# Kernel tuning notes

Hardware: AMD Instinct MI355X
Metric: run time of the kernel (lower is better)

The kernel has to match this reference:

```python
import jax, jax.numpy as jnp
import numpy as np
import math

N = 2048; L = 100; D_IN = 128; D_STATE = 16; D_INNER = 256
MAMBA_DIM = 128; GAT_HID = 64; HEADS = 4; GAT_OUT = 64


def _lin(key, fin, fout, scale=0.02):
    k1, k2 = jax.random.split(key)
    return (jax.random.normal(k1, (fin, fout), jnp.float32) * scale,
            jnp.zeros((fout,), jnp.float32))


def setup_inputs() -> dict:
    key = jax.random.key(0)
    ks = jax.random.split(key, 16)
    temporal_data = jax.random.normal(ks[0], (N, L, D_IN), jnp.float32)
    graph_x = jax.random.normal(ks[1], (N, D_IN), jnp.float32)
    adj = (jax.random.uniform(ks[2], (N, N)) < 0.005).astype(jnp.float32)
    adj_matrix = jnp.maximum(adj, jnp.eye(N, dtype=jnp.float32))
    pos_emb = jax.random.normal(ks[3], (1, 100, D_IN), jnp.float32)
    Wi, bi = _lin(ks[4], D_IN, D_INNER)
    Wg, bg = _lin(ks[5], D_IN, D_INNER)
    A_log = jnp.linspace(math.log(1e-3), math.log(0.1), D_STATE).reshape(1, D_STATE).astype(jnp.float32)
    Wb, bb = _lin(ks[6], D_INNER, D_STATE)
    Wc, bc = _lin(ks[7], D_IN, D_STATE)
    Wo, bo = _lin(ks[8], D_INNER, D_IN)
    Wfc, bfc = _lin(ks[9], D_IN, MAMBA_DIM)
    W1 = jax.random.normal(ks[10], (HEADS, D_IN, GAT_HID), jnp.float32) * 0.05
    a1 = jax.random.normal(ks[11], (HEADS, 2 * GAT_HID), jnp.float32) * 0.05
    W2 = jax.random.normal(ks[12], (1, HEADS * GAT_HID, GAT_OUT), jnp.float32) * 0.05
    a2 = jax.random.normal(ks[13], (1, 2 * GAT_OUT), jnp.float32) * 0.05
    return dict(temporal_data=temporal_data, graph_x=graph_x, adj_matrix=adj_matrix,
                pos_emb=pos_emb, Wi=Wi, bi=bi, Wg=Wg, bg=bg, A_log=A_log,
                Wb=Wb, bb=bb, Wc=Wc, bc=bc, Wo=Wo, bo=bo, Wfc=Wfc, bfc=bfc,
                W1=W1, a1=a1, W2=W2, a2=a2)


def _mamba(x, pos_emb, Wi, bi, Wg, bg, A_log, Wb, bb, Wc, bc, Wo, bo):
    Bt, Ls, _ = x.shape
    x = x + pos_emb[:, :Ls, :]
    x_gated = (x @ Wi + bi) * jax.nn.sigmoid(x @ Wg + bg)   # [B,L,d_inner]
    Bmat = x_gated @ Wb + bb                                 # [B,L,d_state]
    Cmat = x @ Wc + bc                                       # [B,L,d_state]
    A = jnp.exp(0.01 * jnp.exp(A_log))                       # [1,d_state] (dt=0.01)

    def step(h, bc):
        b, c = bc
        h = A * h + b
        return h, h * c

    h0 = jnp.zeros((Bt, A_log.shape[1]), x.dtype)
    _, ys = jax.lax.scan(step, h0, (jnp.swapaxes(Bmat, 0, 1), jnp.swapaxes(Cmat, 0, 1)))
    y = jnp.swapaxes(ys, 0, 1)                               # [B,L,d_state]
    d_inner = Wo.shape[0]
    out_exp = jnp.concatenate(
        [y, jnp.zeros((Bt, Ls, d_inner - y.shape[-1]), x.dtype)], axis=-1)
    return out_exp @ Wo + bo


def _gat_layer(x, adj, W, a, concat):
    # x: [N,Fin], W: [H,Fin,Fout], a: [H,2*Fout]
    F_out = W.shape[2]
    xt = jnp.einsum('nf,hfo->hno', x, W)                     # [H,N,Fout]
    e_src = jnp.einsum('hno,ho->hn', xt, a[:, :F_out])       # a . x_i part
    e_dst = jnp.einsum('hno,ho->hn', xt, a[:, F_out:])       # a . x_j part
    e = jax.nn.leaky_relu(e_src[:, :, None] + e_dst[:, None, :], 0.2)
    e = jnp.where(adj[None, :, :] > 0, e, -jnp.inf)
    att = jax.nn.softmax(e, axis=2)                          # masked entries -> 0
    h_prime = jnp.einsum('hij,hjo->hio', att, xt)            # [H,N,Fout]
    if concat:
        return jnp.transpose(h_prime, (1, 0, 2)).reshape(x.shape[0], -1)
    return h_prime.mean(axis=0)


def reference(temporal_data, graph_x, adj_matrix, pos_emb, Wi, bi, Wg, bg, A_log,
              Wb, bb, Wc, bc, Wo, bo, Wfc, bfc, W1, a1, W2, a2):
    mamba_out = _mamba(temporal_data, pos_emb, Wi, bi, Wg, bg, A_log, Wb, bb, Wc, bc, Wo, bo)
    mamba_features = mamba_out @ Wfc + bfc
    # GAT stack (dropout is identity in eval mode)
    h = _gat_layer(graph_x, adj_matrix, W1, a1, concat=True)
    h = jax.nn.relu(h)
    gat_features = _gat_layer(h, adj_matrix, W2, a2, concat=False)
    return mamba_features, gat_features
```

## Files before the change

kernel.cpp:

```cpp
#include <hip/hip_runtime.h>
#include <hip/hip_bf16.h>

#define N_NODES 2048
#define L_SEQ   100
#define ROWS    (N_NODES * L_SEQ)
#define HEADS   4
#define GHID    64

typedef __attribute__((ext_vector_type(8))) short bf16x8;
typedef __attribute__((ext_vector_type(4))) float floatx4;

__device__ __forceinline__ short f2bf(float f) {
    union { float f; unsigned u; } v; v.f = f;
    return (short)((v.u + 0x8000u) >> 16);
}

constexpr size_t OFF_WCOMB = 0;
constexpr size_t OFF_BCOMB = 2048;
constexpr size_t OFF_AEXP  = 2176;
constexpr size_t OFF_WIGS  = 2192;
constexpr size_t OFF_WBS   = 34960;
constexpr size_t OFF_WCS   = 37008;
constexpr size_t OFF_BM    = 38032;
constexpr size_t OFF_CM    = OFF_BM + (size_t)ROWS * 16;
constexpr size_t OFF_GAT_BIG = OFF_CM + (size_t)ROWS * 16;

constexpr size_t GXT1 = 0;
constexpr size_t GES1 = (size_t)HEADS * N_NODES * GHID;
constexpr size_t GED1 = GES1 + (size_t)HEADS * N_NODES;
constexpr size_t GXT2 = GED1 + (size_t)HEADS * N_NODES;
constexpr size_t GES2 = GXT2 + (size_t)N_NODES * GHID;
constexpr size_t GED2 = GES2 + N_NODES;
constexpr size_t GCNT = GED2 + N_NODES;
constexpr size_t GLIST = GCNT + N_NODES;
constexpr size_t GAT_TOTAL = GLIST + (size_t)N_NODES * 128;

__global__ __launch_bounds__(256) void kA_prep(
    const float* __restrict__ Wo, const float* __restrict__ bo,
    const float* __restrict__ Wfc, const float* __restrict__ bfc,
    const float* __restrict__ A_log,
    const float* __restrict__ Wi, const float* __restrict__ Wg,
    const float* __restrict__ Wb, const float* __restrict__ Wc,
    float* __restrict__ ws) {
    const int b = blockIdx.x;
    if (b < 9) {
        int i = b * 256 + threadIdx.x;
        if (i < 2048) {
            int row = i >> 7, col = i & 127;
            float a = 0.f;
            for (int f = 0; f < 128; f++) a += Wo[row * 128 + f] * Wfc[f * 128 + col];
            ws[OFF_WCOMB + i] = a;
        } else if (i < 2176) {
            int col = i - 2048;
            float acc = bfc[col];
            for (int f = 0; f < 128; f++) acc += bo[f] * Wfc[f * 128 + col];
            ws[OFF_BCOMB + col] = acc;
        } else if (i < 2192) {
            int s = i - 2176;
            ws[OFF_AEXP + s] = expf(0.01f * expf(A_log[s]));
        }
        return;
    }
    int i = (b - 9) * 256 + threadIdx.x;
    short* wigs = (short*)(ws + OFF_WIGS);
    short* wbs  = (short*)(ws + OFF_WBS);
    short* wcs  = (short*)(ws + OFF_WCS);
    if (i < 65536) {
        int j = i & 7, lane = (i >> 3) & 63, ks = (i >> 9) & 3, nt = i >> 11;
        int w = nt >> 3, t = nt & 7;
        int col = w * 64 + (t & 3) * 16 + (lane & 15);
        int k   = ks * 32 + (lane >> 4) * 8 + j;
        float v = (t < 4) ? Wi[k * 256 + col] : Wg[k * 256 + col];
        wigs[i] = f2bf(v);
    } else if (i < 65536 + 4096) {
        int ii = i - 65536;
        int j = ii & 7, lane = (ii >> 3) & 63, ks = ii >> 9;
        int k = ks * 32 + (lane >> 4) * 8 + j, n = lane & 15;
        wbs[ii] = f2bf(Wb[k * 16 + n]);
    } else if (i < 65536 + 4096 + 2048) {
        int ii = i - 65536 - 4096;
        int j = ii & 7, lane = (ii >> 3) & 63, ks = ii >> 9;
        int k = ks * 32 + (lane >> 4) * 8 + j, n = lane & 15;
        wcs[ii] = f2bf(Wc[k * 16 + n]);
    }
}

__global__ __launch_bounds__(512, 3) void k1_mfma(
    const float* __restrict__ temporal, const float* __restrict__ pos,
    const float* __restrict__ bi, const float* __restrict__ bg,
    const float* __restrict__ bb, const float* __restrict__ bc,
    const float* __restrict__ ws, float* __restrict__ Bm, float* __restrict__ Cm) {
    __shared__ short xbf[64][136];
    __shared__ short gbf[64][264];
    const int tid = threadIdx.x, wave = tid >> 6, lane = tid & 63;
    const int m = lane & 15, quad = lane >> 4;
    const int r0 = blockIdx.x * 64;
    const int l0 = r0 % L_SEQ;

#pragma unroll
    for (int i = 0; i < 4; i++) {
        int f4  = i * 512 + tid;
        int row = f4 >> 5;
        int c4  = (f4 & 31) * 4;
        int l = l0 + row; if (l >= L_SEQ) l -= L_SEQ;
        float4 tv = *(const float4*)(temporal + (size_t)(r0 + row) * 128 + c4);
        float4 pv = *(const float4*)(pos + l * 128 + c4);
        short4 sv;
        sv.x = f2bf(tv.x + pv.x); sv.y = f2bf(tv.y + pv.y);
        sv.z = f2bf(tv.z + pv.z); sv.w = f2bf(tv.w + pv.w);
        *(short4*)&xbf[row][c4] = sv;
    }
    __syncthreads();

    const short* Wigs = (const short*)(ws + OFF_WIGS);
    const int wg = wave >> 1, wp = wave & 1;
    const short* bptr[4];
#pragma unroll
    for (int jl = 0; jl < 4; jl++) {
        int ntg = wg * 8 + wp * 2 + (jl & 1) + ((jl >> 1) << 2);
        bptr[jl] = Wigs + (size_t)(ntg * 4 * 64 + lane) * 8;
    }
    floatx4 acc[4][4] = {};
    bf16x8 bcur[4], bnxt[4];
#pragma unroll
    for (int jl = 0; jl < 4; jl++) bcur[jl] = *(const bf16x8*)(bptr[jl]);
#pragma unroll
    for (int ks = 0; ks < 4; ks++) {
        if (ks < 3) {
#pragma unroll
            for (int jl = 0; jl < 4; jl++)
                bnxt[jl] = *(const bf16x8*)(bptr[jl] + (ks + 1) * 512);
        }
#pragma unroll
        for (int mt = 0; mt < 4; mt++) {
            bf16x8 afr = *(const bf16x8*)&xbf[mt * 16 + m][ks * 32 + quad * 8];
#pragma unroll
            for (int jl = 0; jl < 4; jl++)
                acc[mt][jl] = __builtin_amdgcn_mfma_f32_16x16x32_bf16(
                    afr, bcur[jl], acc[mt][jl], 0, 0, 0);
        }
        if (ks < 3) {
#pragma unroll
            for (int jl = 0; jl < 4; jl++) bcur[jl] = bnxt[jl];
        }
    }

    const float NL2E = -1.44269504f;
#pragma unroll
    for (int tp = 0; tp < 2; tp++) {
        int col = wave * 32 + tp * 16 + m;
        float biv = bi[col];
        float bgs = bg[col] * NL2E;
#pragma unroll
        for (int mt = 0; mt < 4; mt++) {
#pragma unroll
            for (int r = 0; r < 4; r++) {
                float li = acc[mt][tp][r] + biv;
                float ex = __builtin_amdgcn_exp2f(fmaf(acc[mt][tp + 2][r], NL2E, bgs));
                float g  = li * __builtin_amdgcn_rcpf(1.f + ex);
                gbf[mt * 16 + quad * 4 + r][col] = f2bf(g);
            }
        }
    }
    __syncthreads();

    if (wave < 4) {
        const short* Wbs = (const short*)(ws + OFF_WBS);
        floatx4 accB = {};
#pragma unroll
        for (int ks = 0; ks < 8; ks++) {
            bf16x8 a = *(const bf16x8*)&gbf[wave * 16 + m][ks * 32 + quad * 8];
            bf16x8 b = *(const bf16x8*)(Wbs + (size_t)(ks * 64 + lane) * 8);
            accB = __builtin_amdgcn_mfma_f32_16x16x32_bf16(a, b, accB, 0, 0, 0);
        }
        float bbv = bb[m];
#pragma unroll
        for (int r = 0; r < 4; r++) {
            int row = r0 + wave * 16 + quad * 4 + r;
            Bm[(size_t)row * 16 + m] = accB[r] + bbv;
        }
    } else {
        const short* Wcs = (const short*)(ws + OFF_WCS);
        const int mt = wave - 4;
        floatx4 accC = {};
#pragma unroll
        for (int ks = 0; ks < 4; ks++) {
            bf16x8 a = *(const bf16x8*)&xbf[mt * 16 + m][ks * 32 + quad * 8];
            bf16x8 b = *(const bf16x8*)(Wcs + (size_t)(ks * 64 + lane) * 8);
            accC = __builtin_amdgcn_mfma_f32_16x16x32_bf16(a, b, accC, 0, 0, 0);
        }
        float bcv = bc[m];
#pragma unroll
        for (int r = 0; r < 4; r++) {
            int row = r0 + mt * 16 + quad * 4 + r;
            Cm[(size_t)row * 16 + m] = accC[r] + bcv;
        }
    }
}

struct __align__(16) ScanSmem { float sb[2][1600]; float sc[2][1600]; };

__device__ __forceinline__ void scan_body(const float* __restrict__ ws,
                                          float* __restrict__ out,
                                          ScanSmem& sm, int bid) {
    const int tid = threadIdx.x;
    const int sub = tid >> 7, t = tid & 127;
    const int n = bid * 2 + sub;
    float* sbp = sm.sb[sub];
    float* scp = sm.sc[sub];
    const float4* Bm4 = (const float4*)(ws + OFF_BM + (size_t)n * 1600);
    const float4* Cm4 = (const float4*)(ws + OFF_CM + (size_t)n * 1600);
#pragma unroll
    for (int i = 0; i < 4; i++) {
        int idx = i * 128 + t;
        if (idx < 400) {
            ((float4*)sbp)[idx] = Bm4[idx];
            ((float4*)scp)[idx] = Cm4[idx];
        }
    }
    float w[16];
#pragma unroll
    for (int s = 0; s < 16; s++) w[s] = ws[OFF_WCOMB + s * 128 + t];
    const float bcb = ws[OFF_BCOMB + t];
    __syncthreads();
    if (t < 16) {
        const int s = t;
        const float As = ws[OFF_AEXP + s];
        float h = 0.f;
#pragma unroll
        for (int lc = 0; lc < 5; lc++) {
            float lb[20], lv[20];
#pragma unroll
            for (int q = 0; q < 20; q++) {
                lb[q] = sbp[(lc * 20 + q) * 16 + s];
                lv[q] = scp[(lc * 20 + q) * 16 + s];
            }
#pragma unroll
            for (int q = 0; q < 20; q++) {
                h = fmaf(As, h, lb[q]);
                sbp[(lc * 20 + q) * 16 + s] = h * lv[q];
            }
        }
    }
    __syncthreads();
    float* op = out + (size_t)n * L_SEQ * 128 + t;
#pragma unroll 2
    for (int l = 0; l < L_SEQ; l++) {
        const float4 y0 = *(const float4*)(sbp + l * 16 + 0);
        const float4 y1 = *(const float4*)(sbp + l * 16 + 4);
        const float4 y2 = *(const float4*)(sbp + l * 16 + 8);
        const float4 y3 = *(const float4*)(sbp + l * 16 + 12);
        float a0 = fmaf(y0.x, w[0], bcb);
        float a1 = y0.y * w[1];
        float a2 = y0.z * w[2];
        float a3 = y0.w * w[3];
        a0 = fmaf(y1.x, w[4], a0); a1 = fmaf(y1.y, w[5], a1);
        a2 = fmaf(y1.z, w[6], a2); a3 = fmaf(y1.w, w[7], a3);
        a0 = fmaf(y2.x, w[8], a0); a1 = fmaf(y2.y, w[9], a1);
        a2 = fmaf(y2.z, w[10], a2); a3 = fmaf(y2.w, w[11], a3);
        a0 = fmaf(y3.x, w[12], a0); a1 = fmaf(y3.y, w[13], a1);
        a2 = fmaf(y3.z, w[14], a2); a3 = fmaf(y3.w, w[15], a3);
        op[(size_t)l * 128] = (a0 + a1) + (a2 + a3);
    }
}

__device__ __forceinline__ void xt1_body(const float* __restrict__ gx,
                                         const float* __restrict__ W1,
                                         const float* __restrict__ a1,
                                         float* __restrict__ gat, int n) {
    const int tid = threadIdx.x;
    const int h = tid >> 6, o = tid & 63;
    float acc = 0.f;
    for (int f = 0; f < 128; f++)
        acc += gx[n * 128 + f] * W1[(h * 128 + f) * 64 + o];
    gat[GXT1 + ((size_t)h * 2048 + n) * 64 + o] = acc;
    float es = acc * a1[h * 128 + o];
    float ed = acc * a1[h * 128 + 64 + o];
#pragma unroll
    for (int off = 32; off > 0; off >>= 1) {
        es += __shfl_down(es, off);
        ed += __shfl_down(ed, off);
    }
    if (o == 0) { gat[GES1 + h * 2048 + n] = es; gat[GED1 + h * 2048 + n] = ed; }
}

__global__ __launch_bounds__(256) void k2_scan(const float* __restrict__ ws,
                                               float* __restrict__ out) {
    __shared__ ScanSmem sm;
    scan_body(ws, out, sm, blockIdx.x);
}

__global__ __launch_bounds__(256) void k4_xt1(const float* __restrict__ gx,
                                              const float* __restrict__ W1,
                                              const float* __restrict__ a1,
                                              float* __restrict__ gat) {
    xt1_body(gx, W1, a1, gat, blockIdx.x);
}

__global__ __launch_bounds__(256) void k24_fused(
    const float* __restrict__ ws, float* __restrict__ out,
    const float* __restrict__ gx, const float* __restrict__ W1,
    const float* __restrict__ a1, float* __restrict__ gat) {
    __shared__ ScanSmem sm;
    if (blockIdx.x < N_NODES / 2) scan_body(ws, out, sm, blockIdx.x);
    else                          xt1_body(gx, W1, a1, gat, blockIdx.x - N_NODES / 2);
}

__global__ __launch_bounds__(256) void k56_att1(const float* __restrict__ adj,
                                                const float* __restrict__ W2,
                                                const float* __restrict__ a2,
                                                float* __restrict__ gat) {
    __shared__ int list[192];
    __shared__ int seg[4][64];
    __shared__ int scnt[4];
    __shared__ float sh1[256];
    __shared__ float sred[4][64];
    const int n = blockIdx.x, tid = threadIdx.x;
    const int h = tid >> 6, o = tid & 63;
    {
        int c = 0;
#pragma unroll
        for (int ch = 0; ch < 8; ch++) {
            int j = h * 512 + ch * 64 + o;
            unsigned long long mask = __ballot(adj[(size_t)n * 2048 + j] > 0.f);
            int pos = c + __popcll(mask & ((1ull << o) - 1ull));
            if ((mask >> o) & 1ull) { if (pos < 64) seg[h][pos] = j; }
            c += (int)__popcll(mask);
        }
        if (o == 0) scnt[h] = (c < 64) ? c : 64;
    }
    __syncthreads();
    const int c0 = scnt[0], c1 = scnt[1], c2 = scnt[2], c3 = scnt[3];
    const int offw = (h > 0 ? c0 : 0) + (h > 1 ? c1 : 0) + (h > 2 ? c2 : 0);
    const int cnt = c0 + c1 + c2 + c3;
    if (o < scnt[h]) list[offw + o] = seg[h][o];
    __syncthreads();
    {
        int* gcnt  = (int*)(gat + GCNT);
        int* glist = (int*)(gat + GLIST);
        if (tid == 0) gcnt[n] = (cnt < 128) ? cnt : 128;
        if (tid < cnt && tid < 128) glist[(size_t)n * 128 + tid] = list[tid];
    }
    {
        const float  es = gat[GES1 + h * 2048 + n];
        const float* ed = gat + GED1 + h * 2048;
        const float* xt = gat + GXT1 + (size_t)h * 2048 * 64;
        float num = 0.f, den = 0.f;
        for (int ii = 0; ii < cnt; ii++) {
            int j = list[ii];
            float e = es + ed[j];
            e = (e > 0.f) ? e : 0.2f * e;
            float wgt = expf(e);
            den += wgt;
            num += wgt * xt[(size_t)j * 64 + o];
        }
        float v = num / den;
        sh1[h * 64 + o] = v > 0.f ? v : 0.f;
    }
    __syncthreads();
    {
        float part = 0.f;
        const int f0 = h * 64;
#pragma unroll 8
        for (int f = 0; f < 64; f++)
            part += sh1[f0 + f] * W2[(f0 + f) * 64 + o];
        sred[h][o] = part;
    }
    __syncthreads();
    if (tid < 64) {
        float xt2v = sred[0][tid] + sred[1][tid] + sred[2][tid] + sred[3][tid];
        gat[GXT2 + (size_t)n * 64 + tid] = xt2v;
        float es = xt2v * a2[tid];
        float ed = xt2v * a2[64 + tid];
#pragma unroll
        for (int off = 32; off > 0; off >>= 1) {
            es += __shfl_down(es, off);
            ed += __shfl_down(ed, off);
        }
        if (tid == 0) { gat[GES2 + n] = es; gat[GED2 + n] = ed; }
    }
}

__global__ __launch_bounds__(256) void k7_att2(const float* __restrict__ gat,
                                               float* __restrict__ gout) {
    __shared__ int list[128];
    __shared__ float snum[4][64];
    __shared__ float sden[4];
    const int n = blockIdx.x, tid = threadIdx.x;
    const int g = tid >> 6, o = tid & 63;
    const int* gcnt  = (const int*)(gat + GCNT);
    const int* glist = (const int*)(gat + GLIST);
    const int mm = gcnt[n];
    if (tid < mm) list[tid] = glist[(size_t)n * 128 + tid];
    __syncthreads();
    const float es = gat[GES2 + n];
    float num = 0.f, den = 0.f;
    for (int ii = g; ii < mm; ii += 4) {
        int j = list[ii];
        float e = es + gat[GED2 + j];
        e = (e > 0.f) ? e : 0.2f * e;
        float wgt = expf(e);
        den += wgt;
        num += wgt * gat[GXT2 + (size_t)j * 64 + o];
    }
    snum[g][o] = num;
    if (o == 0) sden[g] = den;
    __syncthreads();
    if (tid < 64) {
        float nt = snum[0][tid] + snum[1][tid] + snum[2][tid] + snum[3][tid];
        float dt = sden[0] + sden[1] + sden[2] + sden[3];
        gout[(size_t)n * 64 + tid] = nt / dt;
    }
}

extern "C" void kernel_launch(void* const* d_in, const int* in_sizes, int n_in,
                              void* d_out, int out_size, void* d_ws, size_t ws_size,
                              hipStream_t stream) {
    const float* temporal = (const float*)d_in[0];
    const float* graph_x  = (const float*)d_in[1];
    const float* adj      = (const float*)d_in[2];
    const float* pos      = (const float*)d_in[3];
    const float* Wi  = (const float*)d_in[4];
    const float* bi  = (const float*)d_in[5];
    const float* Wg  = (const float*)d_in[6];
    const float* bg  = (const float*)d_in[7];
    const float* A_log = (const float*)d_in[8];
    const float* Wb  = (const float*)d_in[9];
    const float* bb  = (const float*)d_in[10];
    const float* Wc  = (const float*)d_in[11];
    const float* bc  = (const float*)d_in[12];
    const float* Wo  = (const float*)d_in[13];
    const float* bo  = (const float*)d_in[14];
    const float* Wfc = (const float*)d_in[15];
    const float* bfc = (const float*)d_in[16];
    const float* W1  = (const float*)d_in[17];
    const float* a1  = (const float*)d_in[18];
    const float* W2  = (const float*)d_in[19];
    const float* a2  = (const float*)d_in[20];

    float* ws = (float*)d_ws;
    float* out_mamba = (float*)d_out;
    float* out_gat   = out_mamba + (size_t)ROWS * 128;

    const bool big_ws = ws_size >= (OFF_GAT_BIG + GAT_TOTAL) * sizeof(float);
    float* gat = big_ws ? (ws + OFF_GAT_BIG) : (ws + OFF_BM);

    kA_prep<<<289, 256, 0, stream>>>(Wo, bo, Wfc, bfc, A_log, Wi, Wg, Wb, Wc, ws);
    k1_mfma<<<ROWS / 64, 512, 0, stream>>>(temporal, pos, bi, bg, bb, bc, ws,
                                           ws + OFF_BM, ws + OFF_CM);
    if (big_ws) {
        k24_fused<<<N_NODES / 2 + N_NODES, 256, 0, stream>>>(ws, out_mamba,
                                                             graph_x, W1, a1, gat);
    } else {
        k2_scan<<<N_NODES / 2, 256, 0, stream>>>(ws, out_mamba);
        k4_xt1<<<N_NODES, 256, 0, stream>>>(graph_x, W1, a1, gat);
    }
    k56_att1<<<N_NODES, 256, 0, stream>>>(adj, W2, a2, gat);
    k7_att2<<<N_NODES, 256, 0, stream>>>(gat, out_gat);
}
```

Baseline: 335.7 us.

## Regroup kernels: fuse GAT xt1 into MFMA kernel and att1 into scan

Moves the GAT layer-1 projection into the MFMA projection kernel as extra blocks, and fuses the scan with the GAT layer-1 attention kernel, so the independent GAT work overlaps with the Mamba stages and one launch is dropped. It also removes the register double-buffering of B fragments in the MFMA loop and raises the launch-bounds occupancy hint from 3 to 4 blocks. The regrouping relies on the large-workspace path and adds a shared-memory union. Lower register pressure may lose some load latency hiding.

```diff
diff --git a/kernel.cpp b/kernel.cpp
--- a/kernel.cpp
+++ b/kernel.cpp
@@ -85,16 +85,15 @@
     }
 }
 
-__global__ __launch_bounds__(512, 3) void k1_mfma(
+__device__ __forceinline__ void k1_body(
     const float* __restrict__ temporal, const float* __restrict__ pos,
     const float* __restrict__ bi, const float* __restrict__ bg,
     const float* __restrict__ bb, const float* __restrict__ bc,
-    const float* __restrict__ ws, float* __restrict__ Bm, float* __restrict__ Cm) {
-    __shared__ short xbf[64][136];
-    __shared__ short gbf[64][264];
+    const float* __restrict__ ws, float* __restrict__ Bm, float* __restrict__ Cm,
+    short (*xbf)[136], short (*gbf)[264], int bid) {
     const int tid = threadIdx.x, wave = tid >> 6, lane = tid & 63;
     const int m = lane & 15, quad = lane >> 4;
-    const int r0 = blockIdx.x * 64;
+    const int r0 = bid * 64;
     const int l0 = r0 % L_SEQ;
 
 #pragma unroll
@@ -114,35 +113,25 @@
 
     const short* Wigs = (const short*)(ws + OFF_WIGS);
     const int wg = wave >> 1, wp = wave & 1;
-    const short* bptr[4];
-#pragma unroll
-    for (int jl = 0; jl < 4; jl++) {
-        int ntg = wg * 8 + wp * 2 + (jl & 1) + ((jl >> 1) << 2);
-        bptr[jl] = Wigs + (size_t)(ntg * 4 * 64 + lane) * 8;
-    }
     floatx4 acc[4][4] = {};
-    bf16x8 bcur[4], bnxt[4];
-#pragma unroll
-    for (int jl = 0; jl < 4; jl++) bcur[jl] = *(const bf16x8*)(bptr[jl]);
 #pragma unroll
     for (int ks = 0; ks < 4; ks++) {
-        if (ks < 3) {
-#pragma unroll
-            for (int jl = 0; jl < 4; jl++)
-                bnxt[jl] = *(const bf16x8*)(bptr[jl] + (ks + 1) * 512);
-        }
-#pragma unroll
-        for (int mt = 0; mt < 4; mt++) {
-            bf16x8 afr = *(const bf16x8*)&xbf[mt * 16 + m][ks * 32 + quad * 8];
+        bf16x8 bfr[4];
+#pragma unroll
+        for (int jl = 0; jl < 4; jl++) {
+            int ntg = wg * 8 + wp * 2 + (jl & 1) + ((jl >> 1) << 2);
+            bfr[jl] = *(const bf16x8*)(Wigs + (size_t)((ntg * 4 + ks) * 64 + lane) * 8);
+        }
+        bf16x8 afr[4];
+#pragma unroll
+        for (int mt = 0; mt < 4; mt++)
+            afr[mt] = *(const bf16x8*)&xbf[mt * 16 + m][ks * 32 + quad * 8];
+#pragma unroll
+        for (int mt = 0; mt < 4; mt++)
 #pragma unroll
             for (int jl = 0; jl < 4; jl++)
                 acc[mt][jl] = __builtin_amdgcn_mfma_f32_16x16x32_bf16(
-                    afr, bcur[jl], acc[mt][jl], 0, 0, 0);
-        }
-        if (ks < 3) {
-#pragma unroll
-            for (int jl = 0; jl < 4; jl++) bcur[jl] = bnxt[jl];
-        }
+                    afr[mt], bfr[jl], acc[mt][jl], 0, 0, 0);
     }
 
     const float NL2E = -1.44269504f;
@@ -196,6 +185,72 @@
             Cm[(size_t)row * 16 + m] = accC[r] + bcv;
         }
     }
+}
+
+__device__ __forceinline__ void xt1_body512(const float* __restrict__ gx,
+                                            const float* __restrict__ W1,
+                                            const float* __restrict__ a1,
+                                            float* __restrict__ gat, int bid) {
+    const int tid = threadIdx.x;
+    const int nn = tid >> 8, h = (tid >> 6) & 3, o = tid & 63;
+    const int n = bid * 2 + nn;
+    float acc = 0.f;
+    for (int f = 0; f < 128; f++)
+        acc += gx[n * 128 + f] * W1[(h * 128 + f) * 64 + o];
+    gat[GXT1 + ((size_t)h * 2048 + n) * 64 + o] = acc;
+    float es = acc * a1[h * 128 + o];
+    float ed = acc * a1[h * 128 + 64 + o];
+#pragma unroll
+    for (int off = 32; off > 0; off >>= 1) {
+        es += __shfl_down(es, off);
+        ed += __shfl_down(ed, off);
+    }
+    if (o == 0) { gat[GES1 + h * 2048 + n] = es; gat[GED1 + h * 2048 + n] = ed; }
+}
+
+__device__ __forceinline__ void xt1_body(const float* __restrict__ gx,
+                                         const float* __restrict__ W1,
+                                         const float* __restrict__ a1,
+                                         float* __restrict__ gat, int n) {
+    const int tid = threadIdx.x;
+    const int h = tid >> 6, o = tid & 63;
+    float acc = 0.f;
+    for (int f = 0; f < 128; f++)
+        acc += gx[n * 128 + f] * W1[(h * 128 + f) * 64 + o];
+    gat[GXT1 + ((size_t)h * 2048 + n) * 64 + o] = acc;
+    float es = acc * a1[h * 128 + o];
+    float ed = acc * a1[h * 128 + 64 + o];
+#pragma unroll
+    for (int off = 32; off > 0; off >>= 1) {
+        es += __shfl_down(es, off);
+        ed += __shfl_down(ed, off);
+    }
+    if (o == 0) { gat[GES1 + h * 2048 + n] = es; gat[GED1 + h * 2048 + n] = ed; }
+}
+
+__global__ __launch_bounds__(512, 4) void k1_mfma(
+    const float* __restrict__ temporal, const float* __restrict__ pos,
+    const float* __restrict__ bi, const float* __restrict__ bg,
+    const float* __restrict__ bb, const float* __restrict__ bc,
+    const float* __restrict__ ws, float* __restrict__ Bm, float* __restrict__ Cm) {
+    __shared__ short xbf[64][136];
+    __shared__ short gbf[64][264];
+    k1_body(temporal, pos, bi, bg, bb, bc, ws, Bm, Cm, xbf, gbf, blockIdx.x);
+}
+
+__global__ __launch_bounds__(512, 4) void k1x_fused(
+    const float* __restrict__ temporal, const float* __restrict__ pos,
+    const float* __restrict__ bi, const float* __restrict__ bg,
+    const float* __restrict__ bb, const float* __restrict__ bc,
+    const float* __restrict__ ws, float* __restrict__ Bm, float* __restrict__ Cm,
+    const float* __restrict__ gx, const float* __restrict__ W1,
+    const float* __restrict__ a1, float* __restrict__ gat) {
+    __shared__ short xbf[64][136];
+    __shared__ short gbf[64][264];
+    if (blockIdx.x < ROWS / 64)
+        k1_body(temporal, pos, bi, bg, bb, bc, ws, Bm, Cm, xbf, gbf, blockIdx.x);
+    else
+        xt1_body512(gx, W1, a1, gat, blockIdx.x - ROWS / 64);
 }
 
 struct __align__(16) ScanSmem { float sb[2][1600]; float sc[2][1600]; };
@@ -264,58 +319,17 @@
     }
 }
 
-__device__ __forceinline__ void xt1_body(const float* __restrict__ gx,
-                                         const float* __restrict__ W1,
-                                         const float* __restrict__ a1,
-                                         float* __restrict__ gat, int n) {
+struct Att1Smem {
+    int list[192]; int seg[4][64]; int scnt[4];
+    float sh1[256]; float sred[4][64];
+};
+
+__device__ __forceinline__ void att1_body(const float* __restrict__ adj,
+                                          const float* __restrict__ W2,
+                                          const float* __restrict__ a2,
+                                          float* __restrict__ gat,
+                                          Att1Smem& sm, int n) {
     const int tid = threadIdx.x;
-    const int h = tid >> 6, o = tid & 63;
-    float acc = 0.f;
-    for (int f = 0; f < 128; f++)
-        acc += gx[n * 128 + f] * W1[(h * 128 + f) * 64 + o];
-    gat[GXT1 + ((size_t)h * 2048 + n) * 64 + o] = acc;
-    float es = acc * a1[h * 128 + o];
-    float ed = acc * a1[h * 128 + 64 + o];
-#pragma unroll
-    for (int off = 32; off > 0; off >>= 1) {
-        es += __shfl_down(es, off);
-        ed += __shfl_down(ed, off);
-    }
-    if (o == 0) { gat[GES1 + h * 2048 + n] = es; gat[GED1 + h * 2048 + n] = ed; }
-}
-
-__global__ __launch_bounds__(256) void k2_scan(const float* __restrict__ ws,
-                                               float* __restrict__ out) {
-    __shared__ ScanSmem sm;
-    scan_body(ws, out, sm, blockIdx.x);
-}
-
-__global__ __launch_bounds__(256) void k4_xt1(const float* __restrict__ gx,
-                                              const float* __restrict__ W1,
-                                              const float* __restrict__ a1,
-                                              float* __restrict__ gat) {
-    xt1_body(gx, W1, a1, gat, blockIdx.x);
-}
-
-__global__ __launch_bounds__(256) void k24_fused(
-    const float* __restrict__ ws, float* __restrict__ out,
-    const float* __restrict__ gx, const float* __restrict__ W1,
-    const float* __restrict__ a1, float* __restrict__ gat) {
-    __shared__ ScanSmem sm;
-    if (blockIdx.x < N_NODES / 2) scan_body(ws, out, sm, blockIdx.x);
-    else                          xt1_body(gx, W1, a1, gat, blockIdx.x - N_NODES / 2);
-}
-
-__global__ __launch_bounds__(256) void k56_att1(const float* __restrict__ adj,
-                                                const float* __restrict__ W2,
-                                                const float* __restrict__ a2,
-                                                float* __restrict__ gat) {
-    __shared__ int list[192];
-    __shared__ int seg[4][64];
-    __shared__ int scnt[4];
-    __shared__ float sh1[256];
-    __shared__ float sred[4][64];
-    const int n = blockIdx.x, tid = threadIdx.x;
     const int h = tid >> 6, o = tid & 63;
     {
         int c = 0;
@@ -324,22 +338,22 @@
             int j = h * 512 + ch * 64 + o;
             unsigned long long mask = __ballot(adj[(size_t)n * 2048 + j] > 0.f);
             int pos = c + __popcll(mask & ((1ull << o) - 1ull));
-            if ((mask >> o) & 1ull) { if (pos < 64) seg[h][pos] = j; }
+            if ((mask >> o) & 1ull) { if (pos < 64) sm.seg[h][pos] = j; }
             c += (int)__popcll(mask);
         }
-        if (o == 0) scnt[h] = (c < 64) ? c : 64;
-    }
-    __syncthreads();
-    const int c0 = scnt[0], c1 = scnt[1], c2 = scnt[2], c3 = scnt[3];
+        if (o == 0) sm.scnt[h] = (c < 64) ? c : 64;
+    }
+    __syncthreads();
+    const int c0 = sm.scnt[0], c1 = sm.scnt[1], c2 = sm.scnt[2], c3 = sm.scnt[3];
     const int offw = (h > 0 ? c0 : 0) + (h > 1 ? c1 : 0) + (h > 2 ? c2 : 0);
     const int cnt = c0 + c1 + c2 + c3;
-    if (o < scnt[h]) list[offw + o] = seg[h][o];
+    if (o < sm.scnt[h]) sm.list[offw + o] = sm.seg[h][o];
     __syncthreads();
     {
         int* gcnt  = (int*)(gat + GCNT);
         int* glist = (int*)(gat + GLIST);
         if (tid == 0) gcnt[n] = (cnt < 128) ? cnt : 128;
-        if (tid < cnt && tid < 128) glist[(size_t)n * 128 + tid] = list[tid];
+        if (tid < cnt && tid < 128) glist[(size_t)n * 128 + tid] = sm.list[tid];
     }
     {
         const float  es = gat[GES1 + h * 2048 + n];
@@ -347,7 +361,7 @@
         const float* xt = gat + GXT1 + (size_t)h * 2048 * 64;
         float num = 0.f, den = 0.f;
         for (int ii = 0; ii < cnt; ii++) {
-            int j = list[ii];
+            int j = sm.list[ii];
             float e = es + ed[j];
             e = (e > 0.f) ? e : 0.2f * e;
             float wgt = expf(e);
@@ -355,7 +369,7 @@
             num += wgt * xt[(size_t)j * 64 + o];
         }
         float v = num / den;
-        sh1[h * 64 + o] = v > 0.f ? v : 0.f;
+        sm.sh1[h * 64 + o] = v > 0.f ? v : 0.f;
     }
     __syncthreads();
     {
@@ -363,12 +377,12 @@
         const int f0 = h * 64;
 #pragma unroll 8
         for (int f = 0; f < 64; f++)
-            part += sh1[f0 + f] * W2[(f0 + f) * 64 + o];
-        sred[h][o] = part;
+            part += sm.sh1[f0 + f] * W2[(f0 + f) * 64 + o];
+        sm.sred[h][o] = part;
     }
     __syncthreads();
     if (tid < 64) {
-        float xt2v = sred[0][tid] + sred[1][tid] + sred[2][tid] + sred[3][tid];
+        float xt2v = sm.sred[0][tid] + sm.sred[1][tid] + sm.sred[2][tid] + sm.sred[3][tid];
         gat[GXT2 + (size_t)n * 64 + tid] = xt2v;
         float es = xt2v * a2[tid];
         float ed = xt2v * a2[64 + tid];
@@ -379,6 +393,38 @@
         }
         if (tid == 0) { gat[GES2 + n] = es; gat[GED2 + n] = ed; }
     }
+}
+
+__global__ __launch_bounds__(256) void k2_scan(const float* __restrict__ ws,
+                                               float* __restrict__ out) {
+    __shared__ ScanSmem sm;
+    scan_body(ws, out, sm, blockIdx.x);
+}
+
+__global__ __launch_bounds__(256) void k4_xt1(const float* __restrict__ gx,
+                                              const float* __restrict__ W1,
+                                              const float* __restrict__ a1,
+                                              float* __restrict__ gat) {
+    xt1_body(gx, W1, a1, gat, blockIdx.x);
+}
+
+__global__ __launch_bounds__(256) void k56_att1(const float* __restrict__ adj,
+                                                const float* __restrict__ W2,
+                                                const float* __restrict__ a2,
+                                                float* __restrict__ gat) {
+    __shared__ Att1Smem sm;
+    att1_body(adj, W2, a2, gat, sm, blockIdx.x);
+}
+
+union KSASmem { ScanSmem s; Att1Smem a; };
+
+__global__ __launch_bounds__(256) void kSA_fused(
+    const float* __restrict__ ws, float* __restrict__ out,
+    const float* __restrict__ adj, const float* __restrict__ W2,
+    const float* __restrict__ a2, float* __restrict__ gat) {
+    __shared__ KSASmem sm;
+    if (blockIdx.x < N_NODES / 2) scan_body(ws, out, sm.s, blockIdx.x);
+    else                          att1_body(adj, W2, a2, gat, sm.a, blockIdx.x - N_NODES / 2);
 }
 
 __global__ __launch_bounds__(256) void k7_att2(const float* __restrict__ gat,
@@ -446,15 +492,19 @@
     float* gat = big_ws ? (ws + OFF_GAT_BIG) : (ws + OFF_BM);
 
     kA_prep<<<289, 256, 0, stream>>>(Wo, bo, Wfc, bfc, A_log, Wi, Wg, Wb, Wc, ws);
-    k1_mfma<<<ROWS / 64, 512, 0, stream>>>(temporal, pos, bi, bg, bb, bc, ws,
-                                           ws + OFF_BM, ws + OFF_CM);
     if (big_ws) {
-        k24_fused<<<N_NODES / 2 + N_NODES, 256, 0, stream>>>(ws, out_mamba,
-                                                             graph_x, W1, a1, gat);
+        k1x_fused<<<ROWS / 64 + N_NODES / 2, 512, 0, stream>>>(
+            temporal, pos, bi, bg, bb, bc, ws, ws + OFF_BM, ws + OFF_CM,
+            graph_x, W1, a1, gat);
+        kSA_fused<<<N_NODES / 2 + N_NODES, 256, 0, stream>>>(
+            ws, out_mamba, adj, W2, a2, gat);
+        k7_att2<<<N_NODES, 256, 0, stream>>>(gat, out_gat);
     } else {
+        k1_mfma<<<ROWS / 64, 512, 0, stream>>>(temporal, pos, bi, bg, bb, bc, ws,
+                                               ws + OFF_BM, ws + OFF_CM);
         k2_scan<<<N_NODES / 2, 256, 0, stream>>>(ws, out_mamba);
         k4_xt1<<<N_NODES, 256, 0, stream>>>(graph_x, W1, a1, gat);
-    }
-    k56_att1<<<N_NODES, 256, 0, stream>>>(adj, W2, a2, gat);
-    k7_att2<<<N_NODES, 256, 0, stream>>>(gat, out_gat);
-}
+        k56_att1<<<N_NODES, 256, 0, stream>>>(adj, W2, a2, gat);
+        k7_att2<<<N_NODES, 256, 0, stream>>>(gat, out_gat);
+    }
+}
```

Result: no change. 329.1 us (-2.0%).
